# Kernel tuning notes

Measured on AMD Instinct MI355X. Metric: run time of the kernel, lower is better.

Reference implementation:

```python
import jax, jax.numpy as jnp
import numpy as np

N, E = 100000, 1600000
IN, HID, OUT = 128, 64, 64
BN_EPS = 1e-5


def setup_inputs() -> dict:
    key = jax.random.key(0)
    ks = jax.random.split(key, 6)
    x = jax.random.normal(ks[0], (N, IN), dtype=jnp.float32)
    edge_index = jax.random.randint(ks[1], (2, E), 0, N, dtype=jnp.int32)
    W1 = jax.random.normal(ks[2], (IN, HID), dtype=jnp.float32) / np.sqrt(IN).astype(np.float32)
    b1 = jnp.zeros((HID,), jnp.float32)
    bn_weight = jnp.ones((HID,), jnp.float32)
    bn_bias = jnp.zeros((HID,), jnp.float32)
    W2 = jax.random.normal(ks[3], (HID, OUT), dtype=jnp.float32) / np.sqrt(HID).astype(np.float32)
    b2 = jnp.zeros((OUT,), jnp.float32)
    return {"x": x, "edge_index": edge_index, "W1": W1, "b1": b1,
            "bn_weight": bn_weight, "bn_bias": bn_bias, "W2": W2, "b2": b2}


def _gcn_conv(x, W, b, src, dst, deg_inv_sqrt):
    # PyG GCNConv: linear first, then symmetric-normalized aggregation with self-loops.
    h = x @ W                                        # [N, out]
    norm = deg_inv_sqrt[src] * deg_inv_sqrt[dst]     # [E]
    agg = jax.ops.segment_sum(h[src] * norm[:, None], dst, num_segments=h.shape[0])
    # self-loop contribution: norm = 1/deg
    agg = agg + h * (deg_inv_sqrt * deg_inv_sqrt)[:, None]
    return agg + b


def reference(x, edge_index, W1, b1, bn_weight, bn_bias, W2, b2):
    src, dst = edge_index[0], edge_index[1]
    # degree including self-loop (GCNConv add_self_loops=True, edge_weight=1)
    deg = jax.ops.segment_sum(jnp.ones((E,), x.dtype), dst, num_segments=N) + 1.0
    deg_inv_sqrt = jax.lax.rsqrt(deg)
    h = _gcn_conv(x, W1, b1, src, dst, deg_inv_sqrt)
    # BatchNorm1d (training-mode batch statistics, biased variance)
    mean = jnp.mean(h, axis=0)
    var = jnp.var(h, axis=0)
    h = (h - mean) * jax.lax.rsqrt(var + BN_EPS) * bn_weight + bn_bias
    h = jax.nn.relu(h)
    # dropout: inference mode (identity)
    return _gcn_conv(h, W2, b2, src, dst, deg_inv_sqrt)
```

## Files before the change

kernel.cpp:

```cpp
#include <hip/hip_runtime.h>

#define N_NODES 100000
#define E_EDGES 1600000
#define IN_F    128
#define HID_F   64
#define OUT_F   64
#define BN_EPS  1e-5f
#define NBUK    391
#define CHUNK   6250
#define NGBLK   3125
#define NMBLK   1563

typedef __bf16 bf16x8 __attribute__((ext_vector_type(8)));
typedef float  f32x4  __attribute__((ext_vector_type(4)));

__device__ __forceinline__ float bflo(unsigned int u) { return __uint_as_float(u << 16); }
__device__ __forceinline__ float bfhi(unsigned int u) { return __uint_as_float(u & 0xFFFF0000u); }
__device__ __forceinline__ unsigned int pack2bf(float a, float b) {
    unsigned int ua = __float_as_uint(a), ub = __float_as_uint(b);
    ua = (ua + 0x7fffu + ((ua >> 16) & 1u)) >> 16;
    ub = (ub + 0x7fffu + ((ub >> 16) & 1u)) >> 16;
    return ua | (ub << 16);
}
__device__ __forceinline__ unsigned short bf1(float a) {
    unsigned int ua = __float_as_uint(a);
    return (unsigned short)((ua + 0x7fffu + ((ua >> 16) & 1u)) >> 16);
}
#define ADD8(A, u)                                           \
    do {                                                     \
        A[0] += bflo((u).x); A[1] += bfhi((u).x);            \
        A[2] += bflo((u).y); A[3] += bfhi((u).y);            \
        A[4] += bflo((u).z); A[5] += bfhi((u).z);            \
        A[6] += bflo((u).w); A[7] += bfhi((u).w);            \
    } while (0)

__global__ __launch_bounds__(512) void k_chist(const int* __restrict__ dstv,
                                               int* __restrict__ histbuf) {
    __shared__ int h[NBUK];
    const int tid = threadIdx.x;
    const int e0 = blockIdx.x * CHUNK;
    for (int b = tid; b < NBUK; b += 512) h[b] = 0;
    __syncthreads();
    for (int t = tid; t < CHUNK; t += 512)
        atomicAdd(&h[dstv[e0 + t] >> 8], 1);
    __syncthreads();
    for (int b = tid; b < NBUK; b += 512)
        histbuf[blockIdx.x * NBUK + b] = h[b];
}

__global__ __launch_bounds__(256) void k_cscan1(int* __restrict__ histbuf,
                                                int* __restrict__ btot) {
    __shared__ int sh[256];
    const int bkt = blockIdx.x, tid = threadIdx.x;
    int v = histbuf[tid * NBUK + bkt];
    sh[tid] = v;
    __syncthreads();
    for (int off = 1; off < 256; off <<= 1) {
        int t = (tid >= off) ? sh[tid - off] : 0;
        __syncthreads();
        sh[tid] += t;
        __syncthreads();
    }
    histbuf[tid * NBUK + bkt] = sh[tid] - v;
    if (tid == 255) btot[bkt] = sh[255];
}

__global__ __launch_bounds__(512) void k_cscan2(const int* __restrict__ btot,
                                                int* __restrict__ coff) {
    __shared__ int sh[512];
    const int tid = threadIdx.x;
    int v = (tid < NBUK) ? btot[tid] : 0;
    sh[tid] = v;
    __syncthreads();
    for (int off = 1; off < 512; off <<= 1) {
        int t = (tid >= off) ? sh[tid - off] : 0;
        __syncthreads();
        sh[tid] += t;
        __syncthreads();
    }
    if (tid < NBUK) coff[tid] = sh[tid] - v;
    if (tid == 0) coff[NBUK] = E_EDGES;
}

__global__ __launch_bounds__(512) void k_bucket(const int* __restrict__ srcv,
                                                const int* __restrict__ dstv,
                                                const int* __restrict__ histbuf,
                                                const int* __restrict__ coff,
                                                unsigned int* __restrict__ aux) {
    __shared__ int cur[NBUK];
    const int tid = threadIdx.x;
    const int e0 = blockIdx.x * CHUNK;
    for (int i = tid; i < NBUK; i += 512)
        cur[i] = histbuf[blockIdx.x * NBUK + i] + coff[i];
    __syncthreads();
    for (int t = tid; t < CHUNK; t += 512) {
        int d = dstv[e0 + t];
        int s = srcv[e0 + t];
        int pos = atomicAdd(&cur[d >> 8], 1);
        aux[pos] = ((unsigned int)s << 8) | (unsigned int)(d & 255);
    }
}

__global__ __launch_bounds__(256) void k_csrnode(const int* __restrict__ coff,
                                                 const unsigned int* __restrict__ aux,
                                                 int* __restrict__ rowptr,
                                                 float* __restrict__ dis,
                                                 int* __restrict__ csr_src) {
    __shared__ int c0[256], sc[256], cur[256];
    const int tid = threadIdx.x;
    const int n0 = blockIdx.x * 256;
    const int nn = min(256, N_NODES - n0);
    const int estart = coff[blockIdx.x];
    const int eend   = coff[blockIdx.x + 1];
    c0[tid] = 0;
    __syncthreads();
    for (int e = estart + tid; e < eend; e += 256)
        atomicAdd(&c0[aux[e] & 255], 1);
    __syncthreads();
    int v = c0[tid];
    sc[tid] = v;
    __syncthreads();
    for (int off = 1; off < 256; off <<= 1) {
        int t = (tid >= off) ? sc[tid - off] : 0;
        __syncthreads();
        sc[tid] += t;
        __syncthreads();
    }
    int excl = sc[tid] - v;
    if (tid < nn) {
        int p = estart + excl;
        rowptr[n0 + tid] = p;
        cur[tid] = p;
        dis[n0 + tid] = rsqrtf((float)v + 1.0f);
    }
    if (blockIdx.x == NBUK - 1 && tid == 0) rowptr[N_NODES] = E_EDGES;
    __syncthreads();
    for (int e = estart + tid; e < eend; e += 256) {
        unsigned int u = aux[e];
        int pos = atomicAdd(&cur[u & 255], 1);
        csr_src[pos] = (int)(u >> 8);
    }
}

__global__ __launch_bounds__(256) void k_gemm1(const float* __restrict__ x,
                                               const float* __restrict__ W1,
                                               const float* __restrict__ dis,
                                               unsigned short* __restrict__ hs1) {
    __shared__ unsigned short Asb[64 * 136];
    __shared__ unsigned short Btb[64 * 136];
    __shared__ unsigned short Cc[64 * 72];
    __shared__ float disS[64];
    const int tid = threadIdx.x;
    const int r0 = blockIdx.x * 64;

    if (tid < 64) disS[tid] = (r0 + tid < N_NODES) ? dis[r0 + tid] : 0.f;

    const float4* x4 = (const float4*)x;
#pragma unroll
    for (int p = 0; p < 4; ++p) {
        int idx8 = p * 256 + tid;
        int row = idx8 >> 4, c8 = idx8 & 15;
        float4 v0 = make_float4(0.f, 0.f, 0.f, 0.f), v1 = v0;
        if (r0 + row < N_NODES) {
            v0 = x4[(size_t)(r0 + row) * 32 + c8 * 2];
            v1 = x4[(size_t)(r0 + row) * 32 + c8 * 2 + 1];
        }
        uint4 u;
        u.x = pack2bf(v0.x, v0.y); u.y = pack2bf(v0.z, v0.w);
        u.z = pack2bf(v1.x, v1.y); u.w = pack2bf(v1.z, v1.w);
        *(uint4*)&Asb[row * 136 + c8 * 8] = u;
    }
    for (int idx = tid; idx < IN_F * HID_F; idx += 256) {
        int k = idx >> 6, n = idx & 63;
        Btb[n * 136 + k] = bf1(W1[idx]);
    }
    __syncthreads();

    const int wv = tid >> 6, lane = tid & 63;
    const int m = lane & 15, quad = lane >> 4;
    const int arow = wv * 16 + m;
    f32x4 acc[4] = {};
#pragma unroll
    for (int ks = 0; ks < 4; ++ks) {
        int k0 = ks * 32 + quad * 8;
        bf16x8 af = *(const bf16x8*)&Asb[arow * 136 + k0];
#pragma unroll
        for (int c = 0; c < 4; ++c) {
            bf16x8 bfr = *(const bf16x8*)&Btb[(c * 16 + m) * 136 + k0];
            acc[c] = __builtin_amdgcn_mfma_f32_16x16x32_bf16(af, bfr, acc[c], 0, 0, 0);
        }
    }
#pragma unroll
    for (int c = 0; c < 4; ++c)
#pragma unroll
        for (int r = 0; r < 4; ++r) {
            int rl = wv * 16 + quad * 4 + r;
            Cc[rl * 72 + c * 16 + m] = bf1(acc[c][r] * disS[rl]);
        }
    __syncthreads();
#pragma unroll
    for (int p = 0; p < 2; ++p) {
        int idx = p * 256 + tid;
        int row = idx >> 3, c8 = idx & 7;
        if (r0 + row < N_NODES)
            *(uint4*)&hs1[(size_t)(r0 + row) * 64 + c8 * 8] = *(uint4*)&Cc[row * 72 + c8 * 8];
    }
}

__global__ __launch_bounds__(64) void k_gather1(const int* __restrict__ rowptr,
                                                const int* __restrict__ csr_src,
                                                const unsigned short* __restrict__ hsb,
                                                const float* __restrict__ dis,
                                                const float* __restrict__ b1,
                                                unsigned short* __restrict__ aggb,
                                                float* __restrict__ partials) {
    const int tid = threadIdx.x;
    const int g = tid >> 3, q = tid & 7;
    const uint4* __restrict__ hs16 = (const uint4*)hsb;
    const float4 blo = ((const float4*)b1)[q * 2];
    const float4 bhi = ((const float4*)b1)[q * 2 + 1];

    float bsA[4] = {}, bsB[4] = {}, bqA[4] = {}, bqB[4] = {};

#pragma unroll
    for (int jj = 0; jj < 4; ++jj) {
        const int n = blockIdx.x * 32 + jj * 8 + g;
        const int start = rowptr[n], end = rowptr[n + 1];
        float A0[8] = {}, A1[8] = {}, A2[8] = {}, A3[8] = {};
        {
            uint4 u = hs16[(size_t)n * 8 + q];
            ADD8(A0, u);
        }
        int i = start;
        for (; i + 7 < end; i += 8) {
            int s0 = csr_src[i + 0], s1 = csr_src[i + 1];
            int s2 = csr_src[i + 2], s3 = csr_src[i + 3];
            int s4 = csr_src[i + 4], s5 = csr_src[i + 5];
            int s6 = csr_src[i + 6], s7 = csr_src[i + 7];
            uint4 u0 = hs16[(size_t)s0 * 8 + q];
            uint4 u1 = hs16[(size_t)s1 * 8 + q];
            uint4 u2 = hs16[(size_t)s2 * 8 + q];
            uint4 u3 = hs16[(size_t)s3 * 8 + q];
            uint4 u4 = hs16[(size_t)s4 * 8 + q];
            uint4 u5 = hs16[(size_t)s5 * 8 + q];
            uint4 u6 = hs16[(size_t)s6 * 8 + q];
            uint4 u7 = hs16[(size_t)s7 * 8 + q];
            ADD8(A0, u0); ADD8(A1, u1); ADD8(A2, u2); ADD8(A3, u3);
            ADD8(A0, u4); ADD8(A1, u5); ADD8(A2, u6); ADD8(A3, u7);
        }
        if (i + 3 < end) {
            int s0 = csr_src[i + 0], s1 = csr_src[i + 1];
            int s2 = csr_src[i + 2], s3 = csr_src[i + 3];
            uint4 u0 = hs16[(size_t)s0 * 8 + q];
            uint4 u1 = hs16[(size_t)s1 * 8 + q];
            uint4 u2 = hs16[(size_t)s2 * 8 + q];
            uint4 u3 = hs16[(size_t)s3 * 8 + q];
            ADD8(A0, u0); ADD8(A1, u1); ADD8(A2, u2); ADD8(A3, u3);
            i += 4;
        }
        for (; i < end; ++i) {
            uint4 u = hs16[(size_t)csr_src[i] * 8 + q];
            ADD8(A0, u);
        }
        const float d = dis[n];
        float o[8];
        o[0] = fmaf(d, A0[0] + A1[0] + A2[0] + A3[0], blo.x);
        o[1] = fmaf(d, A0[1] + A1[1] + A2[1] + A3[1], blo.y);
        o[2] = fmaf(d, A0[2] + A1[2] + A2[2] + A3[2], blo.z);
        o[3] = fmaf(d, A0[3] + A1[3] + A2[3] + A3[3], blo.w);
        o[4] = fmaf(d, A0[4] + A1[4] + A2[4] + A3[4], bhi.x);
        o[5] = fmaf(d, A0[5] + A1[5] + A2[5] + A3[5], bhi.y);
        o[6] = fmaf(d, A0[6] + A1[6] + A2[6] + A3[6], bhi.z);
        o[7] = fmaf(d, A0[7] + A1[7] + A2[7] + A3[7], bhi.w);
        uint4 ob;
        ob.x = pack2bf(o[0], o[1]); ob.y = pack2bf(o[2], o[3]);
        ob.z = pack2bf(o[4], o[5]); ob.w = pack2bf(o[6], o[7]);
        ((uint4*)aggb)[(size_t)n * 8 + q] = ob;
#pragma unroll
        for (int k = 0; k < 4; ++k) {
            bsA[k] += o[k];     bsB[k] += o[4 + k];
            bqA[k] = fmaf(o[k], o[k], bqA[k]);
            bqB[k] = fmaf(o[4 + k], o[4 + k], bqB[k]);
        }
    }

    __shared__ float4 redA[64], redB[64];
    redA[tid] = make_float4(bsA[0], bsA[1], bsA[2], bsA[3]);
    redB[tid] = make_float4(bsB[0], bsB[1], bsB[2], bsB[3]);
    __syncthreads();
    for (int s = 32; s >= 8; s >>= 1) {
        if (tid < s) {
            redA[tid].x += redA[tid + s].x; redA[tid].y += redA[tid + s].y;
            redA[tid].z += redA[tid + s].z; redA[tid].w += redA[tid + s].w;
            redB[tid].x += redB[tid + s].x; redB[tid].y += redB[tid + s].y;
            redB[tid].z += redB[tid + s].z; redB[tid].w += redB[tid + s].w;
        }
        __syncthreads();
    }
    float4* pr = (float4*)(partials + (size_t)blockIdx.x * 128);
    if (tid < 8) { pr[tid * 2] = redA[tid]; pr[tid * 2 + 1] = redB[tid]; }
    __syncthreads();
    redA[tid] = make_float4(bqA[0], bqA[1], bqA[2], bqA[3]);
    redB[tid] = make_float4(bqB[0], bqB[1], bqB[2], bqB[3]);
    __syncthreads();
    for (int s = 32; s >= 8; s >>= 1) {
        if (tid < s) {
            redA[tid].x += redA[tid + s].x; redA[tid].y += redA[tid + s].y;
            redA[tid].z += redA[tid + s].z; redA[tid].w += redA[tid + s].w;
            redB[tid].x += redB[tid + s].x; redB[tid].y += redB[tid + s].y;
            redB[tid].z += redB[tid + s].z; redB[tid].w += redB[tid + s].w;
        }
        __syncthreads();
    }
    if (tid < 8) { pr[16 + tid * 2] = redA[tid]; pr[16 + tid * 2 + 1] = redB[tid]; }
}

__global__ __launch_bounds__(256) void k_bnfinal(const float* __restrict__ partials,
                                                 float* __restrict__ bnstats) {
    const int c = blockIdx.x;
    const int tid = threadIdx.x;
    float s = 0.f;
    for (int r = tid; r < NGBLK; r += 256)
        s += partials[(size_t)r * 128 + c];
    __shared__ float sh[256];
    sh[tid] = s;
    __syncthreads();
    for (int st = 128; st > 0; st >>= 1) {
        if (tid < st) sh[tid] += sh[tid + st];
        __syncthreads();
    }
    if (tid == 0) bnstats[c] = sh[0];
}

__global__ __launch_bounds__(256) void k_gemm2(const unsigned short* __restrict__ aggb,
                                               const float* __restrict__ W2,
                                               const float* __restrict__ dis,
                                               const float* __restrict__ bnw,
                                               const float* __restrict__ bnb,
                                               const float* __restrict__ bnstats,
                                               unsigned short* __restrict__ hs2) {
    __shared__ unsigned short Ab[64 * 72];
    __shared__ unsigned short Bt2[64 * 72];
    __shared__ unsigned short Cc[64 * 72];
    __shared__ float scale_s[64], shift_s[64], disS[64];
    const int tid = threadIdx.x;
    const int r0 = blockIdx.x * 64;

    if (tid < 64) {
        const float invN = 1.0f / (float)N_NODES;
        float mean = bnstats[tid] * invN;
        float var  = bnstats[64 + tid] * invN - mean * mean;
        float sc   = bnw[tid] * rsqrtf(var + BN_EPS);
        scale_s[tid] = sc;
        shift_s[tid] = fmaf(-mean, sc, bnb[tid]);
        disS[tid] = (r0 + tid < N_NODES) ? dis[r0 + tid] : 0.f;
    }
    for (int idx = tid; idx < HID_F * OUT_F; idx += 256) {
        int k = idx >> 6, n = idx & 63;
        Bt2[n * 72 + k] = bf1(W2[idx]);
    }
    __syncthreads();

    const uint4* a16 = (const uint4*)aggb;
#pragma unroll
    for (int p = 0; p < 2; ++p) {
        int idx = p * 256 + tid;
        int row = idx >> 3, q = idx & 7;
        uint4 u = make_uint4(0, 0, 0, 0);
        if (r0 + row < N_NODES) u = a16[(size_t)(r0 + row) * 8 + q];
        int k0 = q * 8;
        float v[8];
        v[0] = bflo(u.x); v[1] = bfhi(u.x); v[2] = bflo(u.y); v[3] = bfhi(u.y);
        v[4] = bflo(u.z); v[5] = bfhi(u.z); v[6] = bflo(u.w); v[7] = bfhi(u.w);
        uint4 o;
        float w0 = fmaxf(fmaf(v[0], scale_s[k0 + 0], shift_s[k0 + 0]), 0.f);
        float w1 = fmaxf(fmaf(v[1], scale_s[k0 + 1], shift_s[k0 + 1]), 0.f);
        float w2 = fmaxf(fmaf(v[2], scale_s[k0 + 2], shift_s[k0 + 2]), 0.f);
        float w3 = fmaxf(fmaf(v[3], scale_s[k0 + 3], shift_s[k0 + 3]), 0.f);
        float w4 = fmaxf(fmaf(v[4], scale_s[k0 + 4], shift_s[k0 + 4]), 0.f);
        float w5 = fmaxf(fmaf(v[5], scale_s[k0 + 5], shift_s[k0 + 5]), 0.f);
        float w6 = fmaxf(fmaf(v[6], scale_s[k0 + 6], shift_s[k0 + 6]), 0.f);
        float w7 = fmaxf(fmaf(v[7], scale_s[k0 + 7], shift_s[k0 + 7]), 0.f);
        o.x = pack2bf(w0, w1); o.y = pack2bf(w2, w3);
        o.z = pack2bf(w4, w5); o.w = pack2bf(w6, w7);
        *(uint4*)&Ab[row * 72 + q * 8] = o;
    }
    __syncthreads();

    const int wv = tid >> 6, lane = tid & 63;
    const int m = lane & 15, quad = lane >> 4;
    const int arow = wv * 16 + m;
    f32x4 acc[4] = {};
#pragma unroll
    for (int ks = 0; ks < 2; ++ks) {
        int k0 = ks * 32 + quad * 8;
        bf16x8 af = *(const bf16x8*)&Ab[arow * 72 + k0];
#pragma unroll
        for (int c = 0; c < 4; ++c) {
            bf16x8 bfr = *(const bf16x8*)&Bt2[(c * 16 + m) * 72 + k0];
            acc[c] = __builtin_amdgcn_mfma_f32_16x16x32_bf16(af, bfr, acc[c], 0, 0, 0);
        }
    }
#pragma unroll
    for (int c = 0; c < 4; ++c)
#pragma unroll
        for (int r = 0; r < 4; ++r) {
            int rl = wv * 16 + quad * 4 + r;
            Cc[rl * 72 + c * 16 + m] = bf1(acc[c][r] * disS[rl]);
        }
    __syncthreads();
#pragma unroll
    for (int p = 0; p < 2; ++p) {
        int idx = p * 256 + tid;
        int row = idx >> 3, c8 = idx & 7;
        if (r0 + row < N_NODES)
            *(uint4*)&hs2[(size_t)(r0 + row) * 64 + c8 * 8] = *(uint4*)&Cc[row * 72 + c8 * 8];
    }
}

__global__ __launch_bounds__(64) void k_gather2(const int* __restrict__ rowptr,
                                                const int* __restrict__ csr_src,
                                                const unsigned short* __restrict__ hsb,
                                                const float* __restrict__ dis,
                                                const float* __restrict__ b2,
                                                float* __restrict__ out) {
    const int tid = threadIdx.x;
    const int g = tid >> 3, q = tid & 7;
    const uint4* __restrict__ hs16 = (const uint4*)hsb;
    const float4 blo = ((const float4*)b2)[q * 2];
    const float4 bhi = ((const float4*)b2)[q * 2 + 1];

#pragma unroll
    for (int jj = 0; jj < 4; ++jj) {
        const int n = blockIdx.x * 32 + jj * 8 + g;
        const int start = rowptr[n], end = rowptr[n + 1];
        float A0[8] = {}, A1[8] = {}, A2[8] = {}, A3[8] = {};
        {
            uint4 u = hs16[(size_t)n * 8 + q];
            ADD8(A0, u);
        }
        int i = start;
        for (; i + 7 < end; i += 8) {
            int s0 = csr_src[i + 0], s1 = csr_src[i + 1];
            int s2 = csr_src[i + 2], s3 = csr_src[i + 3];
            int s4 = csr_src[i + 4], s5 = csr_src[i + 5];
            int s6 = csr_src[i + 6], s7 = csr_src[i + 7];
            uint4 u0 = hs16[(size_t)s0 * 8 + q];
            uint4 u1 = hs16[(size_t)s1 * 8 + q];
            uint4 u2 = hs16[(size_t)s2 * 8 + q];
            uint4 u3 = hs16[(size_t)s3 * 8 + q];
            uint4 u4 = hs16[(size_t)s4 * 8 + q];
            uint4 u5 = hs16[(size_t)s5 * 8 + q];
            uint4 u6 = hs16[(size_t)s6 * 8 + q];
            uint4 u7 = hs16[(size_t)s7 * 8 + q];
            ADD8(A0, u0); ADD8(A1, u1); ADD8(A2, u2); ADD8(A3, u3);
            ADD8(A0, u4); ADD8(A1, u5); ADD8(A2, u6); ADD8(A3, u7);
        }
        if (i + 3 < end) {
            int s0 = csr_src[i + 0], s1 = csr_src[i + 1];
            int s2 = csr_src[i + 2], s3 = csr_src[i + 3];
            uint4 u0 = hs16[(size_t)s0 * 8 + q];
            uint4 u1 = hs16[(size_t)s1 * 8 + q];
            uint4 u2 = hs16[(size_t)s2 * 8 + q];
            uint4 u3 = hs16[(size_t)s3 * 8 + q];
            ADD8(A0, u0); ADD8(A1, u1); ADD8(A2, u2); ADD8(A3, u3);
            i += 4;
        }
        for (; i < end; ++i) {
            uint4 u = hs16[(size_t)csr_src[i] * 8 + q];
            ADD8(A0, u);
        }
        const float d = dis[n];
        float4 o0, o1;
        o0.x = fmaf(d, A0[0] + A1[0] + A2[0] + A3[0], blo.x);
        o0.y = fmaf(d, A0[1] + A1[1] + A2[1] + A3[1], blo.y);
        o0.z = fmaf(d, A0[2] + A1[2] + A2[2] + A3[2], blo.z);
        o0.w = fmaf(d, A0[3] + A1[3] + A2[3] + A3[3], blo.w);
        o1.x = fmaf(d, A0[4] + A1[4] + A2[4] + A3[4], bhi.x);
        o1.y = fmaf(d, A0[5] + A1[5] + A2[5] + A3[5], bhi.y);
        o1.z = fmaf(d, A0[6] + A1[6] + A2[6] + A3[6], bhi.z);
        o1.w = fmaf(d, A0[7] + A1[7] + A2[7] + A3[7], bhi.w);
        float4* op = (float4*)(out + (size_t)n * OUT_F + q * 8);
        op[0] = o0;
        op[1] = o1;
    }
}

extern "C" void kernel_launch(void* const* d_in, const int* in_sizes, int n_in,
                              void* d_out, int out_size, void* d_ws, size_t ws_size,
                              hipStream_t stream) {
    const float* x   = (const float*)d_in[0];
    const int*   ei  = (const int*)d_in[1];
    const float* W1  = (const float*)d_in[2];
    const float* b1  = (const float*)d_in[3];
    const float* bnw = (const float*)d_in[4];
    const float* bnb = (const float*)d_in[5];
    const float* W2  = (const float*)d_in[6];
    const float* b2  = (const float*)d_in[7];
    float* out = (float*)d_out;

    float* ws = (float*)d_ws;
    float*        dis     = ws;
    int*          rowptr  = (int*)(ws + 100352);
    int*          coff    = (int*)(ws + 200960);
    int*          btot    = (int*)(ws + 201472);
    float*        bnstats = ws + 201984;
    int*          histbuf = (int*)(ws + 202112);
    int*          csr_src = (int*)(ws + 302464);
    float*        bufA    = ws + 1902464;
    float*        bufB    = bufA + (size_t)N_NODES * HID_F;
    unsigned int*   aux  = (unsigned int*)bufA;
    unsigned short* hsb  = (unsigned short*)bufA;
    unsigned short* aggb = (unsigned short*)bufB;
    float* partials = out;

    const int* srcv = ei;
    const int* dstv = ei + E_EDGES;

    k_chist  <<<256, 512, 0, stream>>>(dstv, histbuf);
    k_cscan1 <<<NBUK, 256, 0, stream>>>(histbuf, btot);
    k_cscan2 <<<1, 512, 0, stream>>>(btot, coff);
    k_bucket <<<256, 512, 0, stream>>>(srcv, dstv, histbuf, coff, aux);
    k_csrnode<<<NBUK, 256, 0, stream>>>(coff, aux, rowptr, dis, csr_src);

    k_gemm1  <<<NMBLK, 256, 0, stream>>>(x, W1, dis, hsb);
    k_gather1<<<NGBLK, 64, 0, stream>>>(rowptr, csr_src, hsb, dis, b1, aggb, partials);
    k_bnfinal<<<128, 256, 0, stream>>>(partials, bnstats);
    k_gemm2  <<<NMBLK, 256, 0, stream>>>(aggb, W2, dis, bnw, bnb, bnstats, hsb);
    k_gather2<<<NGBLK, 64, 0, stream>>>(rowptr, csr_src, hsb, dis, b2, out);
}
```

Baseline: 239.8 us.

## Fold bucket prefix scans into bucket kernel and widen CSR node blocks

Removes the two separate scan kernels by transposing the histogram layout so that each bucket-scatter block redundantly computes per-bucket totals, its own block prefix and the global bucket offsets. Block 0 writes the offsets needed later by the CSR build. The CSR node kernel now runs 512 threads per block to process edges with more parallelism. This cuts two launches and their serialization at the cost of redundant scan work in every bucket block.

```diff
diff --git a/kernel.cpp b/kernel.cpp
--- a/kernel.cpp
+++ b/kernel.cpp
@@ -45,54 +45,49 @@
         atomicAdd(&h[dstv[e0 + t] >> 8], 1);
     __syncthreads();
     for (int b = tid; b < NBUK; b += 512)
-        histbuf[blockIdx.x * NBUK + b] = h[b];
-}
-
-__global__ __launch_bounds__(256) void k_cscan1(int* __restrict__ histbuf,
-                                                int* __restrict__ btot) {
-    __shared__ int sh[256];
-    const int bkt = blockIdx.x, tid = threadIdx.x;
-    int v = histbuf[tid * NBUK + bkt];
-    sh[tid] = v;
-    __syncthreads();
-    for (int off = 1; off < 256; off <<= 1) {
-        int t = (tid >= off) ? sh[tid - off] : 0;
-        __syncthreads();
-        sh[tid] += t;
-        __syncthreads();
-    }
-    histbuf[tid * NBUK + bkt] = sh[tid] - v;
-    if (tid == 255) btot[bkt] = sh[255];
-}
-
-__global__ __launch_bounds__(512) void k_cscan2(const int* __restrict__ btot,
-                                                int* __restrict__ coff) {
-    __shared__ int sh[512];
-    const int tid = threadIdx.x;
-    int v = (tid < NBUK) ? btot[tid] : 0;
-    sh[tid] = v;
-    __syncthreads();
-    for (int off = 1; off < 512; off <<= 1) {
-        int t = (tid >= off) ? sh[tid - off] : 0;
-        __syncthreads();
-        sh[tid] += t;
-        __syncthreads();
-    }
-    if (tid < NBUK) coff[tid] = sh[tid] - v;
-    if (tid == 0) coff[NBUK] = E_EDGES;
+        histbuf[b * 256 + blockIdx.x] = h[b];
 }
 
 __global__ __launch_bounds__(512) void k_bucket(const int* __restrict__ srcv,
                                                 const int* __restrict__ dstv,
                                                 const int* __restrict__ histbuf,
-                                                const int* __restrict__ coff,
+                                                int* __restrict__ coff,
                                                 unsigned int* __restrict__ aux) {
+    __shared__ int sh[512];
     __shared__ int cur[NBUK];
     const int tid = threadIdx.x;
-    const int e0 = blockIdx.x * CHUNK;
-    for (int i = tid; i < NBUK; i += 512)
-        cur[i] = histbuf[blockIdx.x * NBUK + i] + coff[i];
-    __syncthreads();
+    const int blk = blockIdx.x;
+    const int e0 = blk * CHUNK;
+
+    int myprefix = 0, total = 0;
+    if (tid < NBUK) {
+        const int4* hb = (const int4*)&histbuf[tid * 256];
+        int acc = 0;
+#pragma unroll 8
+        for (int b4 = 0; b4 < 64; ++b4) {
+            int4 v = hb[b4];
+            int b0 = b4 * 4;
+            if (b0 + 0 == blk) myprefix = acc;  acc += v.x;
+            if (b0 + 1 == blk) myprefix = acc;  acc += v.y;
+            if (b0 + 2 == blk) myprefix = acc;  acc += v.z;
+            if (b0 + 3 == blk) myprefix = acc;  acc += v.w;
+        }
+        total = acc;
+    }
+    sh[tid] = (tid < NBUK) ? total : 0;
+    __syncthreads();
+    for (int off = 1; off < 512; off <<= 1) {
+        int t = (tid >= off) ? sh[tid - off] : 0;
+        __syncthreads();
+        sh[tid] += t;
+        __syncthreads();
+    }
+    int cof = sh[tid] - ((tid < NBUK) ? total : 0);
+    if (tid < NBUK) cur[tid] = cof + myprefix;
+    if (blk == 0 && tid < NBUK) coff[tid] = cof;
+    if (blk == 0 && tid == 0) coff[NBUK] = E_EDGES;
+    __syncthreads();
+
     for (int t = tid; t < CHUNK; t += 512) {
         int d = dstv[e0 + t];
         int s = srcv[e0 + t];
@@ -101,7 +96,7 @@
     }
 }
 
-__global__ __launch_bounds__(256) void k_csrnode(const int* __restrict__ coff,
+__global__ __launch_bounds__(512) void k_csrnode(const int* __restrict__ coff,
                                                  const unsigned int* __restrict__ aux,
                                                  int* __restrict__ rowptr,
                                                  float* __restrict__ dis,
@@ -112,30 +107,32 @@
     const int nn = min(256, N_NODES - n0);
     const int estart = coff[blockIdx.x];
     const int eend   = coff[blockIdx.x + 1];
-    c0[tid] = 0;
-    __syncthreads();
-    for (int e = estart + tid; e < eend; e += 256)
+    if (tid < 256) c0[tid] = 0;
+    __syncthreads();
+    for (int e = estart + tid; e < eend; e += 512)
         atomicAdd(&c0[aux[e] & 255], 1);
     __syncthreads();
-    int v = c0[tid];
-    sc[tid] = v;
+    int v = 0;
+    if (tid < 256) { v = c0[tid]; sc[tid] = v; }
     __syncthreads();
     for (int off = 1; off < 256; off <<= 1) {
-        int t = (tid >= off) ? sc[tid - off] : 0;
-        __syncthreads();
-        sc[tid] += t;
-        __syncthreads();
-    }
-    int excl = sc[tid] - v;
-    if (tid < nn) {
-        int p = estart + excl;
-        rowptr[n0 + tid] = p;
+        int t = 0;
+        if (tid < 256 && tid >= off) t = sc[tid - off];
+        __syncthreads();
+        if (tid < 256) sc[tid] += t;
+        __syncthreads();
+    }
+    if (tid < 256) {
+        int p = estart + sc[tid] - v;
         cur[tid] = p;
-        dis[n0 + tid] = rsqrtf((float)v + 1.0f);
+        if (tid < nn) {
+            rowptr[n0 + tid] = p;
+            dis[n0 + tid] = rsqrtf((float)v + 1.0f);
+        }
     }
     if (blockIdx.x == NBUK - 1 && tid == 0) rowptr[N_NODES] = E_EDGES;
     __syncthreads();
-    for (int e = estart + tid; e < eend; e += 256) {
+    for (int e = estart + tid; e < eend; e += 512) {
         unsigned int u = aux[e];
         int pos = atomicAdd(&cur[u & 255], 1);
         csr_src[pos] = (int)(u >> 8);
@@ -503,9 +500,8 @@
     float*        dis     = ws;
     int*          rowptr  = (int*)(ws + 100352);
     int*          coff    = (int*)(ws + 200960);
-    int*          btot    = (int*)(ws + 201472);
-    float*        bnstats = ws + 201984;
-    int*          histbuf = (int*)(ws + 202112);
+    float*        bnstats = ws + 201472;
+    int*          histbuf = (int*)(ws + 201984);
     int*          csr_src = (int*)(ws + 302464);
     float*        bufA    = ws + 1902464;
     float*        bufB    = bufA + (size_t)N_NODES * HID_F;
@@ -518,10 +514,8 @@
     const int* dstv = ei + E_EDGES;
 
     k_chist  <<<256, 512, 0, stream>>>(dstv, histbuf);
-    k_cscan1 <<<NBUK, 256, 0, stream>>>(histbuf, btot);
-    k_cscan2 <<<1, 512, 0, stream>>>(btot, coff);
     k_bucket <<<256, 512, 0, stream>>>(srcv, dstv, histbuf, coff, aux);
-    k_csrnode<<<NBUK, 256, 0, stream>>>(coff, aux, rowptr, dis, csr_src);
+    k_csrnode<<<NBUK, 512, 0, stream>>>(coff, aux, rowptr, dis, csr_src);
 
     k_gemm1  <<<NMBLK, 256, 0, stream>>>(x, W1, dis, hsb);
     k_gather1<<<NGBLK, 64, 0, stream>>>(rowptr, csr_src, hsb, dis, b1, aggb, partials);
```

New measurement: 241.5 us. About the same (+0.7%).
